# Kernel optimization log

Measured on AMD Instinct MI355X. Metric: run time of the kernel, lower is better.

The kernel has to match this reference:

```python
import jax, jax.numpy as jnp
import numpy as np

DIM = 1024
HEADS = 16
DIM_HEAD = 64
INNER = HEADS * DIM_HEAD  # 1024


def setup_inputs() -> dict:
    key = jax.random.key(0)
    ks = jax.random.split(key, 5)
    B, N = 4, 2048
    x = jax.random.normal(ks[0], (B, N, DIM), dtype=jnp.float32)
    # nn.Linear weights stored as [out, in]; we keep [in, out] for x @ W
    s = 1.0 / np.sqrt(DIM)
    Wq = jax.random.uniform(ks[1], (DIM, INNER), jnp.float32, -s, s)
    Wkv = jax.random.uniform(ks[2], (DIM, 2 * INNER), jnp.float32, -s, s)
    so = 1.0 / np.sqrt(INNER)
    Wo = jax.random.uniform(ks[3], (INNER, DIM), jnp.float32, -so, so)
    bo = jax.random.uniform(ks[4], (DIM,), jnp.float32, -so, so)
    return {"x": x, "Wq": Wq, "Wkv": Wkv, "Wo": Wo, "bo": bo}


def reference(x, Wq, Wkv, Wo, bo):
    B, N, _ = x.shape
    scale = DIM_HEAD ** -0.5
    q = x @ Wq                      # [B, N, INNER]
    kv = x @ Wkv                    # [B, N, 2*INNER]
    k, v = jnp.split(kv, 2, axis=-1)

    def split_heads(t):
        return t.reshape(B, N, HEADS, DIM_HEAD).transpose(0, 2, 1, 3)  # b h n d

    q, k, v = map(split_heads, (q, k, v))
    dots = jnp.einsum('bhid,bhjd->bhij', q, k) * scale
    # causal mask: positions j > i filled with -inf
    causal = jnp.triu(jnp.ones((N, N), dtype=bool), k=1)
    dots = jnp.where(causal, -jnp.inf, dots)
    attn = jax.nn.softmax(dots, axis=-1)
    out = jnp.einsum('bhij,bhjd->bhid', attn, v)
    out = out.transpose(0, 2, 1, 3).reshape(B, N, INNER)
    return out @ Wo + bo
```

## Files before the change

### kernel.cpp

```cpp
#include <hip/hip_runtime.h>
#include <hip/hip_bf16.h>
#include <math.h>

typedef __attribute__((ext_vector_type(8))) short bf16x8;
typedef __attribute__((ext_vector_type(4))) float f32x4;

static __device__ inline ushort f2bf(float f) {
    union { float f; unsigned u; } v; v.f = f;
    unsigned r = (v.u + 0x7fff + ((v.u >> 16) & 1)) >> 16;
    return (ushort)r;
}

#define GLD_LDS(g, l) \
    __builtin_amdgcn_global_load_lds( \
        (const __attribute__((address_space(1))) void*)(g), \
        (__attribute__((address_space(3))) void*)(l), 16, 0, 0)

__global__ __launch_bounds__(256) void convert_x(
    const float* __restrict__ x, ushort* __restrict__ xb)
{
    const size_t i = ((size_t)blockIdx.x * 256 + threadIdx.x) * 8;
    float4 a = *(const float4*)(x + i);
    float4 b = *(const float4*)(x + i + 4);
    bf16x8 t;
    t[0] = (short)f2bf(a.x); t[1] = (short)f2bf(a.y);
    t[2] = (short)f2bf(a.z); t[3] = (short)f2bf(a.w);
    t[4] = (short)f2bf(b.x); t[5] = (short)f2bf(b.y);
    t[6] = (short)f2bf(b.z); t[7] = (short)f2bf(b.w);
    *(bf16x8*)(xb + i) = t;
}

__global__ __launch_bounds__(256) void prep_w(
    const float* __restrict__ Wq, const float* __restrict__ Wkv,
    const float* __restrict__ Wo, ushort* __restrict__ Wt)
{
    const int w = threadIdx.x >> 6;
    const int lane = threadIdx.x & 63;
    const int tile = blockIdx.x * 4 + w;
    const int r0 = (tile >> 4) << 6;
    const int k0 = (tile & 15) << 6;

    const float* src; int ld, c0;
    if (r0 < 1024)      { src = Wq;  ld = 1024; c0 = r0; }
    else if (r0 < 3072) { src = Wkv; ld = 2048; c0 = r0 - 1024; }
    else                { src = Wo;  ld = 1024; c0 = r0 - 3072; }

    ushort v[64];
    #pragma unroll
    for (int k = 0; k < 64; ++k)
        v[k] = f2bf(src[(size_t)(k0 + k) * ld + c0 + lane]);

    ushort* dst = Wt + (size_t)(r0 + lane) * 1024 + k0;
    #pragma unroll
    for (int k = 0; k < 64; k += 8) {
        bf16x8 t;
        #pragma unroll
        for (int j = 0; j < 8; ++j) t[j] = (short)v[k + j];
        *(bf16x8*)(dst + k) = t;
    }
}

#define STG_A(t) { ushort* d_ = &As[(t) & 1][ldst];                            \
    GLD_LDS(aS0 + (size_t)(t) * 64, d_);                                       \
    GLD_LDS(aS1 + (size_t)(t) * 64, d_ + 64 * 64); }
#define STG_B1(t) { ushort* d_ = &Bs[(t) & 1][ldst];                           \
    GLD_LDS(bS0 + (size_t)(t) * 64, d_);                                       \
    GLD_LDS(bS1 + (size_t)(t) * 64, d_ + 64 * 64); }
#define STG_B2(t) { ushort* d_ = &Bs[(t) & 1][128 * 64 + ldst];                \
    GLD_LDS(bS2 + (size_t)(t) * 64, d_);                                       \
    GLD_LDS(bS3 + (size_t)(t) * 64, d_ + 64 * 64); }

#define GEMM_PIPE(Aptr, Btptr, NXT, NWG)                                       \
    __shared__ ushort As[2][128 * 64];                                         \
    __shared__ ushort Bs[2][256 * 64];                                         \
    const int tid = threadIdx.x;                                               \
    const int lane = tid & 63;                                                 \
    const int w = tid >> 6;                                                    \
    const int l15 = lane & 15;                                                 \
    const int quad = lane >> 4;                                                \
    const int wm = w >> 2, wn = w & 3;                                         \
    const int cx = l15 & 7;                                                    \
    const int lin = blockIdx.y * (NXT) + blockIdx.x;                           \
    const int wg = (lin & 7) * ((NWG) >> 3) + (lin >> 3);                      \
    const int rowBase = (wg / (NXT)) * 128;                                    \
    const int colBase = (wg % (NXT)) * 256;                                    \
    const int sr = tid >> 3, sc = tid & 7;                                     \
    const int ldst = sr * 64 + sc * 8;                                         \
    const ushort* aS0 = (Aptr) + (size_t)(rowBase + sr) * 1024 + ((sc ^ (sr & 7)) << 3); \
    const ushort* aS1 = aS0 + (size_t)64 * 1024;                               \
    const ushort* bS0 = (Btptr) + (size_t)(colBase + sr) * 1024 + ((sc ^ (sr & 7)) << 3); \
    const ushort* bS1 = bS0 + (size_t)64 * 1024;                               \
    const ushort* bS2 = bS0 + (size_t)128 * 1024;                              \
    const ushort* bS3 = bS0 + (size_t)192 * 1024;                              \
    f32x4 acc[4][4];                                                           \
    _Pragma("unroll")                                                          \
    for (int i_ = 0; i_ < 4; ++i_)                                             \
        _Pragma("unroll")                                                      \
        for (int j_ = 0; j_ < 4; ++j_) acc[i_][j_] = (f32x4){0.f, 0.f, 0.f, 0.f}; \
    STG_A(0) STG_B1(0) STG_B2(0) STG_B1(1) STG_B2(1)                           \
    asm volatile("s_waitcnt vmcnt(4)" ::: "memory");                           \
    __builtin_amdgcn_s_barrier();                                              \
    asm volatile("" ::: "memory");                                             \
    _Pragma("unroll 1")                                                        \
    for (int u = 0; u < 16; ++u) {                                             \
        const ushort* aRd = &As[u & 1][(wm * 64 + l15) * 64];                  \
        const ushort* bRd = &Bs[u & 1][(wn * 64 + l15) * 64];                  \
        const int c0 = (quad ^ cx) << 3, c1 = ((4 | quad) ^ cx) << 3;          \
        bf16x8 bF0[4], bF1[4];                                                 \
        _Pragma("unroll")                                                      \
        for (int ni = 0; ni < 4; ++ni) {                                       \
            bF0[ni] = *(const bf16x8*)(bRd + ni * 1024 + c0);                  \
            bF1[ni] = *(const bf16x8*)(bRd + ni * 1024 + c1);                  \
        }                                                                      \
        bf16x8 a0 = *(const bf16x8*)(aRd + c0);                                \
        bf16x8 a1 = *(const bf16x8*)(aRd + c1);                                \
        if (u + 1 < 16) { STG_A(u + 1) }                                       \
        __builtin_amdgcn_s_barrier();                                          \
        asm volatile("s_waitcnt lgkmcnt(0)" ::: "memory");                     \
        __builtin_amdgcn_sched_barrier(0);                                     \
        __builtin_amdgcn_s_setprio(1);                                         \
        _Pragma("unroll")                                                      \
        for (int ni = 0; ni < 4; ++ni) {                                       \
            acc[0][ni] = __builtin_amdgcn_mfma_f32_16x16x32_bf16(a0, bF0[ni], acc[0][ni], 0, 0, 0); \
            acc[0][ni] = __builtin_amdgcn_mfma_f32_16x16x32_bf16(a1, bF1[ni], acc[0][ni], 0, 0, 0); \
        }                                                                      \
        __builtin_amdgcn_s_setprio(0);                                         \
        __builtin_amdgcn_s_barrier();                                          \
        asm volatile("" ::: "memory");                                         \
        _Pragma("unroll")                                                      \
        for (int q = 1; q < 4; ++q) {                                          \
            bf16x8 aa = *(const bf16x8*)(aRd + q * 1024 + c0);                 \
            bf16x8 ab = *(const bf16x8*)(aRd + q * 1024 + c1);                 \
            if (q == 1 && u + 2 < 16) { STG_B1(u + 2) }                        \
            if (q == 2 && u + 2 < 16) { STG_B2(u + 2) }                        \
            __builtin_amdgcn_s_barrier();                                      \
            asm volatile("s_waitcnt lgkmcnt(0)" ::: "memory");                 \
            __builtin_amdgcn_sched_barrier(0);                                 \
            __builtin_amdgcn_s_setprio(1);                                     \
            _Pragma("unroll")                                                  \
            for (int ni = 0; ni < 4; ++ni) {                                   \
                acc[q][ni] = __builtin_amdgcn_mfma_f32_16x16x32_bf16(aa, bF0[ni], acc[q][ni], 0, 0, 0); \
                acc[q][ni] = __builtin_amdgcn_mfma_f32_16x16x32_bf16(ab, bF1[ni], acc[q][ni], 0, 0, 0); \
            }                                                                  \
            __builtin_amdgcn_s_setprio(0);                                     \
            if (q == 3) {                                                      \
                if (u < 14) { asm volatile("s_waitcnt vmcnt(4)" ::: "memory"); } \
                else        { asm volatile("s_waitcnt vmcnt(0)" ::: "memory"); } \
            }                                                                  \
            __builtin_amdgcn_s_barrier();                                      \
            asm volatile("" ::: "memory");                                     \
        }                                                                      \
    }

__global__ __launch_bounds__(512, 2) void gemm_qkv(
    const ushort* __restrict__ A, const ushort* __restrict__ Bt,
    ushort* __restrict__ Qb, ushort* __restrict__ Kb, ushort* __restrict__ Vt)
{
    GEMM_PIPE(A, Bt, 12, 768)

    const int seg = colBase >> 10;
    if (seg == 2) {
        #pragma unroll
        for (int mi = 0; mi < 4; ++mi) {
            #pragma unroll
            for (int ni = 0; ni < 4; ++ni) {
                const int c = (colBase + wn*64 + ni*16 + l15) & 1023;
                const int h = c >> 6, d = c & 63;
                const int m = rowBase + wm*64 + mi*16 + quad*4;
                const int b = m >> 11, nn = m & 2047;
                ushort4 v;
                v.x = f2bf(acc[mi][ni][0]); v.y = f2bf(acc[mi][ni][1]);
                v.z = f2bf(acc[mi][ni][2]); v.w = f2bf(acc[mi][ni][3]);
                *(ushort4*)(Vt + ((size_t)(b*16 + h)*64 + d)*2048 + nn) = v;
            }
        }
    } else {
        ushort* dst = seg ? Kb : Qb;
        const float sc2 = seg ? 1.0f : 0.18033688011112042f;
        #pragma unroll
        for (int mi = 0; mi < 4; ++mi) {
            #pragma unroll
            for (int ni = 0; ni < 4; ++ni) {
                const int c = (colBase + wn*64 + ni*16 + l15) & 1023;
                const int h = c >> 6, d = c & 63;
                #pragma unroll
                for (int r = 0; r < 4; ++r) {
                    const int m = rowBase + wm*64 + mi*16 + quad*4 + r;
                    const int b = m >> 11, nn = m & 2047;
                    dst[((((size_t)b*16 + h)*2048 + nn) << 6) + d] = f2bf(acc[mi][ni][r] * sc2);
                }
            }
        }
    }
}

__global__ __launch_bounds__(512, 2) void gemm_out(
    const ushort* __restrict__ A, const ushort* __restrict__ Bt,
    const float* __restrict__ bo, float* __restrict__ out)
{
    GEMM_PIPE(A, Bt, 4, 256)

    #pragma unroll
    for (int mi = 0; mi < 4; ++mi) {
        #pragma unroll
        for (int ni = 0; ni < 4; ++ni) {
            const int n = colBase + wn*64 + ni*16 + l15;
            const float bb = bo[n];
            #pragma unroll
            for (int r = 0; r < 4; ++r) {
                const int m = rowBase + wm*64 + mi*16 + quad*4 + r;
                out[(size_t)m * 1024 + n] = acc[mi][ni][r] + bb;
            }
        }
    }
}

__device__ __forceinline__ bf16x8 lds_frag(const ushort* S, int row, int chunk) {
    return *(const bf16x8*)(S + row * 64 + ((chunk ^ (row & 7)) << 3));
}

__global__ __launch_bounds__(256, 2) void flash_mfma(
    const ushort* __restrict__ Qb,
    const ushort* __restrict__ Kb,
    const ushort* __restrict__ Vt,
    ushort* __restrict__ Ob)
{
    __shared__ ushort Ks[2][4096];
    __shared__ ushort Vs[2][4096];
    __shared__ ushort PsAll[4][32][72];

    const int tid = threadIdx.x;
    const int w = tid >> 6;
    const int lane = tid & 63;
    const int l15 = lane & 15;
    const int quad = lane >> 4;
    ushort (*Ps)[72] = PsAll[w];

    const int blk = blockIdx.x;
    const int bh = ((blk & 7) << 3) | ((blk >> 3) & 7);
    const int qt = 15 - (blk >> 6);
    const int nt = 2 * qt + 2;
    const int rb0 = (qt << 7) + w * 32;

    const int sr0 = tid >> 3, sr1 = sr0 + 32;
    const int cg0 = (tid & 7) ^ (sr0 & 7);
    const int cg1 = (tid & 7) ^ (sr1 & 7);
    const ushort* kgb = Kb + (size_t)bh * 131072;
    const ushort* vgb = Vt + (size_t)bh * 131072;

    bf16x8 qf[2][2];
    #pragma unroll
    for (int mi = 0; mi < 2; ++mi) {
        const ushort* qp = Qb + ((size_t)bh * 2048 + rb0 + mi*16 + l15) * 64 + quad * 8;
        qf[mi][0] = *(const bf16x8*)qp;
        qf[mi][1] = *(const bf16x8*)(qp + 32);
    }

    bf16x8 bones;
    #pragma unroll
    for (int j = 0; j < 8; ++j) bones[j] = (short)0x3F80;

    float m_r[2];
    f32x4 o[2][4], lacc[2];
    #pragma unroll
    for (int mi = 0; mi < 2; ++mi) {
        m_r[mi] = -INFINITY;
        lacc[mi] = (f32x4){0.f, 0.f, 0.f, 0.f};
        #pragma unroll
        for (int nb = 0; nb < 4; ++nb) o[mi][nb] = (f32x4){0.f, 0.f, 0.f, 0.f};
    }

    GLD_LDS(kgb + sr0*64 + cg0*8, &Ks[0][tid*8]);
    GLD_LDS(kgb + sr1*64 + cg1*8, &Ks[0][tid*8 + 2048]);
    GLD_LDS(vgb + (size_t)sr0*2048 + cg0*8, &Vs[0][tid*8]);
    GLD_LDS(vgb + (size_t)sr1*2048 + cg1*8, &Vs[0][tid*8 + 2048]);

    for (int t = 0; t < nt; ++t) {
        __syncthreads();
        const int cur = t & 1;
        if (t + 1 < nt) {
            const int jn = t + 1;
            ushort* kd = &Ks[cur ^ 1][tid * 8];
            ushort* vd = &Vs[cur ^ 1][tid * 8];
            GLD_LDS(kgb + (size_t)jn*4096 + sr0*64 + cg0*8, kd);
            GLD_LDS(kgb + (size_t)jn*4096 + sr1*64 + cg1*8, kd + 2048);
            GLD_LDS(vgb + (size_t)sr0*2048 + jn*64 + cg0*8, vd);
            GLD_LDS(vgb + (size_t)sr1*2048 + jn*64 + cg1*8, vd + 2048);
        }
        const int j0 = t << 6;
        if (j0 > rb0 + 31) continue;

        const ushort* Ksb = Ks[cur];
        const ushort* Vsb = Vs[cur];

        f32x4 St[2][4];
        #pragma unroll
        for (int kb = 0; kb < 4; ++kb) {
            bf16x8 ka = lds_frag(Ksb, kb*16 + l15, quad);
            bf16x8 kc = lds_frag(Ksb, kb*16 + l15, quad + 4);
            #pragma unroll
            for (int mi = 0; mi < 2; ++mi) {
                f32x4 s = (f32x4){0.f, 0.f, 0.f, 0.f};
                s = __builtin_amdgcn_mfma_f32_16x16x32_bf16(ka, qf[mi][0], s, 0, 0, 0);
                s = __builtin_amdgcn_mfma_f32_16x16x32_bf16(kc, qf[mi][1], s, 0, 0, 0);
                St[mi][kb] = s;
            }
        }

        #pragma unroll
        for (int mi = 0; mi < 2; ++mi) {
            const int qrow = rb0 + mi*16 + l15;
            if (j0 + 63 > rb0 + mi*16) {
                #pragma unroll
                for (int kb = 0; kb < 4; ++kb) {
                    const int kbase = j0 + kb*16 + quad*4;
                    #pragma unroll
                    for (int r = 0; r < 4; ++r)
                        if (kbase + r > qrow) St[mi][kb][r] = -INFINITY;
                }
            }
            f32x4 mv = St[mi][0];
            #pragma unroll
            for (int kb = 1; kb < 4; ++kb)
                #pragma unroll
                for (int r = 0; r < 4; ++r) mv[r] = fmaxf(mv[r], St[mi][kb][r]);
            float mx = fmaxf(fmaxf(mv[0], mv[1]), fmaxf(mv[2], mv[3]));
            mx = fmaxf(mx, __shfl_xor(mx, 16));
            mx = fmaxf(mx, __shfl_xor(mx, 32));
            const float mold = m_r[mi];
            const float mnew = fmaxf(mold, mx);
            if (__any(mnew > mold)) {
                m_r[mi] = mnew;
                const float corr = __builtin_amdgcn_exp2f(mold - mnew);
                float ct[4];
                #pragma unroll
                for (int r = 0; r < 4; ++r) ct[r] = __shfl(corr, quad*4 + r);
                #pragma unroll
                for (int r = 0; r < 4; ++r) lacc[mi][r] *= ct[r];
                #pragma unroll
                for (int nb = 0; nb < 4; ++nb)
                    #pragma unroll
                    for (int r = 0; r < 4; ++r) o[mi][nb][r] *= ct[r];
            }
            #pragma unroll
            for (int kb = 0; kb < 4; ++kb)
                #pragma unroll
                for (int r = 0; r < 4; ++r)
                    St[mi][kb][r] = __builtin_amdgcn_exp2f(St[mi][kb][r] - mnew);
            #pragma unroll
            for (int kb = 0; kb < 4; ++kb) {
                union { float f; unsigned u; } c0, c1, c2, c3;
                c0.f = St[mi][kb][0]; c1.f = St[mi][kb][1];
                c2.f = St[mi][kb][2]; c3.f = St[mi][kb][3];
                uint2 pk;
                pk.x = (c0.u >> 16) | (c1.u & 0xFFFF0000u);
                pk.y = (c2.u >> 16) | (c3.u & 0xFFFF0000u);
                *(uint2*)&Ps[mi*16 + l15][kb*16 + quad*4] = pk;
            }
        }

        bf16x8 pf[2][2];
        #pragma unroll
        for (int mi = 0; mi < 2; ++mi) {
            pf[mi][0] = *(const bf16x8*)&Ps[mi*16 + l15][quad * 8];
            pf[mi][1] = *(const bf16x8*)&Ps[mi*16 + l15][32 + quad * 8];
        }
        #pragma unroll
        for (int mi = 0; mi < 2; ++mi) {
            lacc[mi] = __builtin_amdgcn_mfma_f32_16x16x32_bf16(pf[mi][0], bones, lacc[mi], 0, 0, 0);
            lacc[mi] = __builtin_amdgcn_mfma_f32_16x16x32_bf16(pf[mi][1], bones, lacc[mi], 0, 0, 0);
        }
        #pragma unroll
        for (int nb = 0; nb < 4; ++nb) {
            bf16x8 va = lds_frag(Vsb, nb*16 + l15, quad);
            bf16x8 vc = lds_frag(Vsb, nb*16 + l15, quad + 4);
            #pragma unroll
            for (int mi = 0; mi < 2; ++mi) {
                o[mi][nb] = __builtin_amdgcn_mfma_f32_16x16x32_bf16(pf[mi][0], va, o[mi][nb], 0, 0, 0);
                o[mi][nb] = __builtin_amdgcn_mfma_f32_16x16x32_bf16(pf[mi][1], vc, o[mi][nb], 0, 0, 0);
            }
        }
    }

    const int b = bh >> 4, h = bh & 15;
    #pragma unroll
    for (int mi = 0; mi < 2; ++mi)
        #pragma unroll
        for (int r = 0; r < 4; ++r) {
            const int ig = rb0 + mi*16 + quad*4 + r;
            const float inv = 1.f / lacc[mi][r];
            ushort* op = Ob + ((size_t)(b * 2048 + ig)) * 1024 + h * 64 + l15;
            #pragma unroll
            for (int nb = 0; nb < 4; ++nb)
                op[nb * 16] = f2bf(o[mi][nb][r] * inv);
        }
}

extern "C" void kernel_launch(void* const* d_in, const int* in_sizes, int n_in,
                              void* d_out, int out_size, void* d_ws, size_t ws_size,
                              hipStream_t stream) {
    const float* x   = (const float*)d_in[0];
    const float* Wq  = (const float*)d_in[1];
    const float* Wkv = (const float*)d_in[2];
    const float* Wo  = (const float*)d_in[3];
    const float* bo  = (const float*)d_in[4];
    float* out = (float*)d_out;

    const size_t SEG = (size_t)8388608 * 2;
    char* ws = (char*)d_ws;
    ushort* xb = (ushort*)(ws);
    ushort* Qb = (ushort*)(ws + SEG);
    ushort* Kb = (ushort*)(ws + SEG * 2);
    ushort* Vt = (ushort*)(ws + SEG * 3);
    ushort* Ob = (ushort*)(ws + SEG * 4);
    ushort* Wt = (ushort*)(ws + SEG * 5);

    convert_x<<<dim3(4096), 256, 0, stream>>>(x, xb);
    prep_w<<<dim3(256), 256, 0, stream>>>(Wq, Wkv, Wo, Wt);
    gemm_qkv<<<dim3(12, 64), 512, 0, stream>>>(xb, Wt, Qb, Kb, Vt);
    flash_mfma<<<dim3(1024), 256, 0, stream>>>(Qb, Kb, Vt, Ob);
    gemm_out<<<dim3(4, 64), 512, 0, stream>>>(Ob, Wt + (size_t)3072 * 1024, bo, out);
}
```

Measured before the change: 248.6 us.

## Restructure GEMM main loop into two phases with fewer barriers

```diff
diff --git a/kernel.cpp b/kernel.cpp
--- a/kernel.cpp
+++ b/kernel.cpp
@@ -106,14 +106,17 @@
         const ushort* aRd = &As[u & 1][(wm * 64 + l15) * 64];                  \
         const ushort* bRd = &Bs[u & 1][(wn * 64 + l15) * 64];                  \
         const int c0 = (quad ^ cx) << 3, c1 = ((4 | quad) ^ cx) << 3;          \
+                                  \
         bf16x8 bF0[4], bF1[4];                                                 \
         _Pragma("unroll")                                                      \
         for (int ni = 0; ni < 4; ++ni) {                                       \
             bF0[ni] = *(const bf16x8*)(bRd + ni * 1024 + c0);                  \
             bF1[ni] = *(const bf16x8*)(bRd + ni * 1024 + c1);                  \
         }                                                                      \
-        bf16x8 a0 = *(const bf16x8*)(aRd + c0);                                \
-        bf16x8 a1 = *(const bf16x8*)(aRd + c1);                                \
+        bf16x8 a00 = *(const bf16x8*)(aRd + c0);                               \
+        bf16x8 a01 = *(const bf16x8*)(aRd + c1);                               \
+        bf16x8 a10 = *(const bf16x8*)(aRd + 1024 + c0);                        \
+        bf16x8 a11 = *(const bf16x8*)(aRd + 1024 + c1);                        \
         if (u + 1 < 16) { STG_A(u + 1) }                                       \
         __builtin_amdgcn_s_barrier();                                          \
         asm volatile("s_waitcnt lgkmcnt(0)" ::: "memory");                     \
@@ -121,35 +124,42 @@
         __builtin_amdgcn_s_setprio(1);                                         \
         _Pragma("unroll")                                                      \
         for (int ni = 0; ni < 4; ++ni) {                                       \
-            acc[0][ni] = __builtin_amdgcn_mfma_f32_16x16x32_bf16(a0, bF0[ni], acc[0][ni], 0, 0, 0); \
-            acc[0][ni] = __builtin_amdgcn_mfma_f32_16x16x32_bf16(a1, bF1[ni], acc[0][ni], 0, 0, 0); \
+            acc[0][ni] = __builtin_amdgcn_mfma_f32_16x16x32_bf16(a00, bF0[ni], acc[0][ni], 0, 0, 0); \
+            acc[0][ni] = __builtin_amdgcn_mfma_f32_16x16x32_bf16(a01, bF1[ni], acc[0][ni], 0, 0, 0); \
+        }                                                                      \
+        _Pragma("unroll")                                                      \
+        for (int ni = 0; ni < 4; ++ni) {                                       \
+            acc[1][ni] = __builtin_amdgcn_mfma_f32_16x16x32_bf16(a10, bF0[ni], acc[1][ni], 0, 0, 0); \
+            acc[1][ni] = __builtin_amdgcn_mfma_f32_16x16x32_bf16(a11, bF1[ni], acc[1][ni], 0, 0, 0); \
         }                                                                      \
         __builtin_amdgcn_s_setprio(0);                                         \
         __builtin_amdgcn_s_barrier();                                          \
         asm volatile("" ::: "memory");                                         \
-        _Pragma("unroll")                                                      \
-        for (int q = 1; q < 4; ++q) {                                          \
-            bf16x8 aa = *(const bf16x8*)(aRd + q * 1024 + c0);                 \
-            bf16x8 ab = *(const bf16x8*)(aRd + q * 1024 + c1);                 \
-            if (q == 1 && u + 2 < 16) { STG_B1(u + 2) }                        \
-            if (q == 2 && u + 2 < 16) { STG_B2(u + 2) }                        \
-            __builtin_amdgcn_s_barrier();                                      \
-            asm volatile("s_waitcnt lgkmcnt(0)" ::: "memory");                 \
-            __builtin_amdgcn_sched_barrier(0);                                 \
-            __builtin_amdgcn_s_setprio(1);                                     \
-            _Pragma("unroll")                                                  \
-            for (int ni = 0; ni < 4; ++ni) {                                   \
-                acc[q][ni] = __builtin_amdgcn_mfma_f32_16x16x32_bf16(aa, bF0[ni], acc[q][ni], 0, 0, 0); \
-                acc[q][ni] = __builtin_amdgcn_mfma_f32_16x16x32_bf16(ab, bF1[ni], acc[q][ni], 0, 0, 0); \
-            }                                                                  \
-            __builtin_amdgcn_s_setprio(0);                                     \
-            if (q == 3) {                                                      \
-                if (u < 14) { asm volatile("s_waitcnt vmcnt(4)" ::: "memory"); } \
-                else        { asm volatile("s_waitcnt vmcnt(0)" ::: "memory"); } \
-            }                                                                  \
-            __builtin_amdgcn_s_barrier();                                      \
-            asm volatile("" ::: "memory");                                     \
+                                            \
+        bf16x8 a20 = *(const bf16x8*)(aRd + 2 * 1024 + c0);                    \
+        bf16x8 a21 = *(const bf16x8*)(aRd + 2 * 1024 + c1);                    \
+        bf16x8 a30 = *(const bf16x8*)(aRd + 3 * 1024 + c0);                    \
+        bf16x8 a31 = *(const bf16x8*)(aRd + 3 * 1024 + c1);                    \
+        if (u + 2 < 16) { STG_B1(u + 2) STG_B2(u + 2) }                        \
+        __builtin_amdgcn_s_barrier();                                          \
+        asm volatile("s_waitcnt lgkmcnt(0)" ::: "memory");                     \
+        __builtin_amdgcn_sched_barrier(0);                                     \
+        __builtin_amdgcn_s_setprio(1);                                         \
+        _Pragma("unroll")                                                      \
+        for (int ni = 0; ni < 4; ++ni) {                                       \
+            acc[2][ni] = __builtin_amdgcn_mfma_f32_16x16x32_bf16(a20, bF0[ni], acc[2][ni], 0, 0, 0); \
+            acc[2][ni] = __builtin_amdgcn_mfma_f32_16x16x32_bf16(a21, bF1[ni], acc[2][ni], 0, 0, 0); \
         }                                                                      \
+        _Pragma("unroll")                                                      \
+        for (int ni = 0; ni < 4; ++ni) {                                       \
+            acc[3][ni] = __builtin_amdgcn_mfma_f32_16x16x32_bf16(a30, bF0[ni], acc[3][ni], 0, 0, 0); \
+            acc[3][ni] = __builtin_amdgcn_mfma_f32_16x16x32_bf16(a31, bF1[ni], acc[3][ni], 0, 0, 0); \
+        }                                                                      \
+        __builtin_amdgcn_s_setprio(0);                                         \
+        if (u < 14) { asm volatile("s_waitcnt vmcnt(4)" ::: "memory"); }       \
+        else        { asm volatile("s_waitcnt vmcnt(0)" ::: "memory"); }       \
+        __builtin_amdgcn_s_barrier();                                          \
+        asm volatile("" ::: "memory");                                         \
     }
 
 __global__ __launch_bounds__(512, 2) void gemm_qkv(
```

After: 245.8 us. No clear change (-1.1%).
